# Kernel tuning notes

Measured on AMD Instinct MI355X. Metric: run time of the kernel, lower is better.

The kernel has to match this reference:

```python
import jax, jax.numpy as jnp
import numpy as np

TEM = 6  # forward hardcodes Tem=6 for index building; init default Tem=6 for weights


def _build_index(H, W, Tem):
    # Faithful port of _build_matrix_index: row edges per phase, col edges per phase,
    # then cross-phase edges linking corresponding pixels of adjacent phases.
    raw = jnp.arange(W, dtype=jnp.int32)[None, :] + jnp.arange(H, dtype=jnp.int32)[:, None] * W  # [H,W]
    pw = W // Tem
    phases = [raw[:, i * pw:(i + 1) * pw] for i in range(Tem)]
    rows = [jnp.stack([p[:-1, :], p[1:, :]], axis=2).reshape(-1, 2) for p in phases]
    cols = [jnp.stack([p[:, :-1], p[:, 1:]], axis=2).reshape(-1, 2) for p in phases]
    cross = [jnp.stack([phases[i], phases[i + 1]], axis=2).reshape(-1, 2) for i in range(Tem - 1)]
    return jnp.concatenate(rows + cols + cross, axis=0)  # [E,2]


def _build_weight_norm2(fm, Tem):
    # Faithful port of _build_feature_weight_norm2_distance, INCLUDING the original
    # per-phase [row,col] interleaved ordering (which differs from the index ordering).
    B, D, H, W = fm.shape
    pw = W // Tem
    phases = [fm[:, :, :, i * pw:(i + 1) * pw] for i in range(Tem)]
    ws = []
    for p in phases:
        wr = ((p[:, :, :-1, :] - p[:, :, 1:, :]) ** 2).sum(axis=1).reshape(B, -1)
        wc = ((p[:, :, :, :-1] - p[:, :, :, 1:]) ** 2).sum(axis=1).reshape(B, -1)
        ws.extend([wr, wc])
    for i in range(Tem - 1):
        ws.append(((phases[i] - phases[i + 1]) ** 2).sum(axis=1).reshape(B, -1))
    return jnp.concatenate(ws, axis=1)  # [B,E]


def _mst_single(u, v, w, V):
    # Vectorized Boruvka MST with pointer-jumping union-find (jit-compatible,
    # fixed round count >= ceil(log2 V)). Ties broken by a globally unique edge rank.
    E = u.shape[0]
    order = jnp.argsort(w)  # stable -> unique rank per edge
    rank = jnp.zeros(E, jnp.int32).at[order].set(jnp.arange(E, dtype=jnp.int32))
    n_rounds = int(np.ceil(np.log2(max(V, 2)))) + 1
    idx_v = jnp.arange(V, dtype=jnp.int32)

    def round_fn(carry, _):
        comp, mask = carry
        cu, cv = comp[u], comp[v]
        active = cu != cv
        key = jnp.where(active, rank, E)  # E = sentinel 'no edge'
        mk = jnp.minimum(jax.ops.segment_min(key, cu, num_segments=V),
                         jax.ops.segment_min(key, cv, num_segments=V))  # min rank per component
        has = mk < E
        sel = order[jnp.clip(mk, 0, E - 1)]  # chosen edge index per component
        a, b = cu[sel], cv[sel]
        other = jnp.where(a == idx_v, b, a)
        parent = jnp.where(has, other, idx_v)
        # break mutual 2-cycles: smaller-index component becomes root
        gp = parent[parent]
        parent = jnp.where((gp == idx_v) & (idx_v < parent), idx_v, parent)
        # full path compression via pointer jumping
        parent = jax.lax.while_loop(lambda p: jnp.any(p[p] != p), lambda p: p[p], parent)
        comp = parent[comp]
        mask = mask.at[jnp.where(has, sel, E)].set(True)  # slot E is scratch
        return (comp, mask), None

    comp0 = jnp.arange(V, dtype=jnp.int32)
    mask0 = jnp.zeros(E + 1, dtype=bool)
    (comp, mask), _ = jax.lax.scan(round_fn, (comp0, mask0), None, length=n_rounds)
    mask = mask[:E]
    # grid graph is connected -> exactly V-1 selected edges; emit sorted edge ids
    tree = jnp.sort(jnp.where(mask, jnp.arange(E, dtype=jnp.int32), E))[: V - 1]
    return tree  # [V-1] int32


def setup_inputs() -> dict:
    key = jax.random.key(0)
    guide_in = jax.random.normal(key, (4, 64, 288, 432), dtype=jnp.float32)
    return {"guide_in": guide_in}


def reference(guide_in):
    B, C, H, W = guide_in.shape
    V = H * W
    index = _build_index(H, W, TEM)  # [E,2], same for every batch element
    weight = _build_weight_norm2(guide_in, TEM)  # [B,E]
    u, v = index[:, 0], index[:, 1]
    tree = jax.vmap(lambda ww: _mst_single(u, v, ww, V))(weight)  # [B, V-1]
    return tree
```

## Files before the change

### kernel.cpp

```cpp
#include <hip/hip_runtime.h>
#include <cstdint>
#include <cstddef>

#define NB 4
#define NC 64
#define HH 288
#define WW 432
#define PW 72
#define NV (HH*WW)
#define R_PER ((HH-1)*PW)
#define C_PER (HH*(PW-1))
#define X_PER (HH*PW)
#define PAIRW (R_PER + C_PER)
#define ROWS_TOT (6*R_PER)
#define ROWCOL (6*PAIRW)
#define NE (ROWCOL + 5*X_PER)
#define NEB ((NE + 255)/256)
#define EPT 4
#define NEB4 ((NE + 1023)/1024)
#define NTREE (NV-1)
#define NROUNDS 18
#define CHUNK 4096
#define NCHUNK ((NE + CHUNK - 1)/CHUNK)
#define CSTR 32
#define SLB 128

typedef unsigned long long ull;

__device__ __forceinline__ void index_uv(int e, int& u, int& v) {
    if (e < ROWS_TOT) {
        int t = e / R_PER, l = e - t * R_PER;
        int h = l / PW, x = l - h * PW;
        u = h * WW + t * PW + x; v = u + WW;
    } else if (e < ROWCOL) {
        int q = e - ROWS_TOT;
        int t = q / C_PER, l = q - t * C_PER;
        int h = l / (PW-1), x = l - h * (PW-1);
        u = h * WW + t * PW + x; v = u + 1;
    } else {
        int q = e - ROWCOL;
        int t = q / X_PER, l = q - t * X_PER;
        int h = l / PW, x = l - h * PW;
        u = h * WW + t * PW + x; v = u + PW;
    }
}

__device__ __forceinline__ int rootOf2(const int* __restrict__ par, int c, int p) {
    while (true) {
        if (p == c) return c;
        int pp = par[p];
        if (pp == c) return c < p ? c : p;
        c = p; p = pp;
    }
}

__global__ __launch_bounds__(256) void init_kernel(int* comp, int* parent,
                                                   ull* minkey, unsigned char* mask,
                                                   int* cnt, int* found, int* done) {
    int i = blockIdx.x * 256 + threadIdx.x;
    int b = blockIdx.y;
    if (i < NV) {
        comp[(size_t)b*NV + i] = i;
        parent[(size_t)b*NV + i] = i;
        minkey[(size_t)b*NV + i] = ~0ULL;
    }
    if (i < NE) mask[(size_t)b*NE + i] = 0;
    if (b == 0 && i < 2*NB*CSTR) cnt[i] = 0;
    if (b == 0 && i < NB) { found[i] = 1; found[NB + i] = 0; done[i] = 0; }
}

__global__ __launch_bounds__(256) void key0_kernel(const float* __restrict__ fm,
                                                   ull* __restrict__ keys,
                                                   ull* __restrict__ minkey) {
    int i = blockIdx.x * 256 + threadIdx.x;
    int b = blockIdx.y;
    if (i >= NV) return;
    int h = i / WW, x = i - h * WW;
    int t = x / PW, xr = x - t * PW;
    bool hv = (h < HH-1);
    bool hh = (xr < PW-1);
    bool hx = (x < WW-PW);
    int ov = hv ? WW : 0;
    int oh = hh ? 1  : 0;
    int ox = hx ? PW : 0;
    const float* base = fm + (size_t)b * NC * NV + i;
    float sv = 0.f, sh_ = 0.f, sx = 0.f;
    #pragma unroll 8
    for (int ch = 0; ch < NC; ++ch) {
        const float* p = base + (size_t)ch * NV;
        float f0 = p[0];
        float dv = f0 - p[ov];
        float dh = f0 - p[oh];
        float dx = f0 - p[ox];
        sv += dv * dv; sh_ += dh * dh; sx += dx * dx;
    }
    ull* mk = minkey + (size_t)b * NV;
    ull* ky = keys + (size_t)b * NE;
    if (hv) {
        int e = t * PAIRW + h * PW + xr;
        ull k = ((ull)__float_as_uint(sv) << 32) | (unsigned int)e;
        ky[e] = k;
        int u, v; index_uv(e, u, v);
        atomicMin(&mk[u], k); atomicMin(&mk[v], k);
    }
    if (hh) {
        int e = t * PAIRW + R_PER + h * (PW-1) + xr;
        ull k = ((ull)__float_as_uint(sh_) << 32) | (unsigned int)e;
        ky[e] = k;
        int u, v; index_uv(e, u, v);
        atomicMin(&mk[u], k); atomicMin(&mk[v], k);
    }
    if (hx) {
        int e = ROWCOL + t * X_PER + h * PW + xr;
        ull k = ((ull)__float_as_uint(sx) << 32) | (unsigned int)e;
        ky[e] = k;
        int u, v; index_uv(e, u, v);
        atomicMin(&mk[u], k); atomicMin(&mk[v], k);
    }
}

__global__ __launch_bounds__(256) void scan_full_kernel(const ull* __restrict__ keys,
                                                        int* __restrict__ comp,
                                                        const int* __restrict__ parent,
                                                        ull* __restrict__ minkey,
                                                        int* __restrict__ list0,
                                                        int* __restrict__ cnt,
                                                        int* __restrict__ fCur) {
    const int tid = threadIdx.x;
    const int b = blockIdx.y;
    const int ebase = blockIdx.x * (256 * EPT) + tid;
    const size_t offV = (size_t)b * NV;
    const int* par = parent + offV;
    int* cmp = comp + offV;
    ull* mk = minkey + offV;
    const ull* ky = keys + (size_t)b * NE;

    int e[EPT], uu[EPT], vv[EPT], cu0[EPT], cv0[EPT], pu0[EPT], pv0[EPT];
    ull k[EPT];
    bool valid[EPT], live[EPT];
    #pragma unroll
    for (int j = 0; j < EPT; ++j) {
        e[j] = ebase + j * 256;
        valid[j] = e[j] < NE;
        int u = 0, v = 0;
        if (valid[j]) index_uv(e[j], u, v);
        uu[j] = u; vv[j] = v;
    }
    #pragma unroll
    for (int j = 0; j < EPT; ++j) {
        cu0[j] = valid[j] ? cmp[uu[j]] : 0;
        cv0[j] = valid[j] ? cmp[vv[j]] : 0;
        k[j]   = valid[j] ? ky[e[j]] : 0;
    }
    #pragma unroll
    for (int j = 0; j < EPT; ++j) {
        pu0[j] = valid[j] ? par[cu0[j]] : 0;
        pv0[j] = valid[j] ? par[cv0[j]] : 0;
    }
    #pragma unroll
    for (int j = 0; j < EPT; ++j) {
        live[j] = false;
        if (valid[j]) {
            int cu = rootOf2(par, cu0[j], pu0[j]);
            int cv = rootOf2(par, cv0[j], pv0[j]);
            if (cu0[j] != cu) cmp[uu[j]] = cu;
            if (cv0[j] != cv) cmp[vv[j]] = cv;
            live[j] = (cu != cv);
            if (live[j]) {
                if (k[j] < mk[cu]) atomicMin(&mk[cu], k[j]);
                if (k[j] < mk[cv]) atomicMin(&mk[cv], k[j]);
            }
        }
    }
    __shared__ int s_w[4];
    __shared__ int s_bcnt;
    __shared__ int s_gb;
    const int lane = tid & 63;
    const int wid = tid >> 6;
    ull wl[EPT]; int wcnt = 0;
    #pragma unroll
    for (int j = 0; j < EPT; ++j) { wl[j] = __ballot(live[j] ? 1 : 0); wcnt += __popcll(wl[j]); }
    if (tid == 0) s_bcnt = 0;
    __syncthreads();
    if (lane == 0) s_w[wid] = wcnt ? atomicAdd(&s_bcnt, wcnt) : 0;
    __syncthreads();
    if (tid == 0 && s_bcnt) {
        s_gb = atomicAdd(&cnt[b * CSTR], s_bcnt);
        fCur[b] = 1;
    }
    __syncthreads();
    int pre = 0;
    #pragma unroll
    for (int j = 0; j < EPT; ++j) {
        if (live[j]) {
            int pos = s_gb + s_w[wid] + pre + __popcll(wl[j] & ((1ull << lane) - 1));
            list0[(size_t)b * NE + pos] = e[j];
        }
        pre += __popcll(wl[j]);
    }
}

__global__ __launch_bounds__(256) void scan_list_kernel(const ull* __restrict__ keys,
                                                        int* __restrict__ comp,
                                                        const int* __restrict__ parent,
                                                        ull* __restrict__ minkey,
                                                        int* __restrict__ list0,
                                                        int* __restrict__ list1,
                                                        int* __restrict__ cnt,
                                                        int rpar,
                                                        int* __restrict__ fCur,
                                                        const int* __restrict__ done) {
    const int b = blockIdx.y;
    if (done[b]) return;
    const int tid = threadIdx.x;
    const int n = cnt[rpar * NB * CSTR + b * CSTR];
    int* cw = &cnt[(rpar ^ 1) * NB * CSTR + b * CSTR];
    const int* lr = (rpar ? list1 : list0) + (size_t)b * NE;
    int* lw = (rpar ? list0 : list1) + (size_t)b * NE;
    const size_t offV = (size_t)b * NV;
    const int* par = parent + offV;
    int* cmp = comp + offV;
    ull* mk = minkey + offV;
    const ull* ky = keys + (size_t)b * NE;

    const int stride = SLB * 256 * EPT;
    const int nIter = (n + stride - 1) / stride;
    const int lane = tid & 63;
    const int wid = tid >> 6;
    __shared__ int s_w[4];
    __shared__ int s_bcnt;
    __shared__ int s_gb;

    for (int it = 0; it < nIter; ++it) {
        const int ibase = it * stride + blockIdx.x * (256 * EPT) + tid;
        int e[EPT], uu[EPT], vv[EPT], cu0[EPT], cv0[EPT], pu0[EPT], pv0[EPT];
        ull k[EPT];
        bool valid[EPT], live[EPT];
        #pragma unroll
        for (int j = 0; j < EPT; ++j) {
            int i = ibase + j * 256;
            valid[j] = i < n;
            e[j] = valid[j] ? lr[i] : 0;
        }
        #pragma unroll
        for (int j = 0; j < EPT; ++j) {
            int u = 0, v = 0;
            if (valid[j]) index_uv(e[j], u, v);
            uu[j] = u; vv[j] = v;
        }
        #pragma unroll
        for (int j = 0; j < EPT; ++j) {
            cu0[j] = valid[j] ? cmp[uu[j]] : 0;
            cv0[j] = valid[j] ? cmp[vv[j]] : 0;
            k[j]   = valid[j] ? ky[e[j]] : 0;
        }
        #pragma unroll
        for (int j = 0; j < EPT; ++j) {
            pu0[j] = valid[j] ? par[cu0[j]] : 0;
            pv0[j] = valid[j] ? par[cv0[j]] : 0;
        }
        #pragma unroll
        for (int j = 0; j < EPT; ++j) {
            live[j] = false;
            if (valid[j]) {
                int cu = rootOf2(par, cu0[j], pu0[j]);
                int cv = rootOf2(par, cv0[j], pv0[j]);
                if (cu0[j] != cu) cmp[uu[j]] = cu;
                if (cv0[j] != cv) cmp[vv[j]] = cv;
                live[j] = (cu != cv);
                if (live[j]) {
                    if (k[j] < mk[cu]) atomicMin(&mk[cu], k[j]);
                    if (k[j] < mk[cv]) atomicMin(&mk[cv], k[j]);
                }
            }
        }
        ull wl[EPT]; int wcnt = 0;
        #pragma unroll
        for (int j = 0; j < EPT; ++j) { wl[j] = __ballot(live[j] ? 1 : 0); wcnt += __popcll(wl[j]); }
        if (tid == 0) s_bcnt = 0;
        __syncthreads();
        if (lane == 0) s_w[wid] = wcnt ? atomicAdd(&s_bcnt, wcnt) : 0;
        __syncthreads();
        if (tid == 0 && s_bcnt) {
            s_gb = atomicAdd(cw, s_bcnt);
            fCur[b] = 1;
        }
        __syncthreads();
        int pre = 0;
        #pragma unroll
        for (int j = 0; j < EPT; ++j) {
            if (live[j]) {
                int pos = s_gb + s_w[wid] + pre + __popcll(wl[j] & ((1ull << lane) - 1));
                lw[pos] = e[j];
            }
            pre += __popcll(wl[j]);
        }
    }
}

__global__ __launch_bounds__(256) void select_kernel(const int* __restrict__ comp,
                                                     int* __restrict__ parent,
                                                     ull* __restrict__ minkey,
                                                     unsigned char* __restrict__ mask,
                                                     const int* __restrict__ foundCur,
                                                     int* __restrict__ foundNext,
                                                     int* __restrict__ done,
                                                     int* __restrict__ cnt,
                                                     int zpar) {
    int gid = blockIdx.x * 256 + threadIdx.x;
    int b = blockIdx.y;
    int fc = foundCur[b];
    if (gid == 0) {
        foundNext[b] = 0;
        cnt[zpar * NB * CSTR + b * CSTR] = 0;
        if (fc == 0) done[b] = 1;
    }
    if (fc == 0) return;
    int c0 = gid * 4;
    if (c0 >= NV) return;
    size_t off = (size_t)b * NV;
    ulonglong4 kv = *reinterpret_cast<const ulonglong4*>(minkey + off + c0);
    int4 pv = *reinterpret_cast<const int4*>(parent + off + c0);
    ull kk[4] = {kv.x, kv.y, kv.z, kv.w};
    int pold[4] = {pv.x, pv.y, pv.z, pv.w};
    #pragma unroll
    for (int j = 0; j < 4; ++j) {
        int c = c0 + j;
        int pr = c;
        if (kk[j] != ~0ULL) {
            minkey[off + c] = ~0ULL;
            int e = (int)(kk[j] & 0xffffffffu);
            mask[(size_t)b * NE + e] = 1;
            int u, v; index_uv(e, u, v);
            int cu = comp[off + u], cv = comp[off + v];
            pr = (cu == c) ? cv : cu;
        }
        if (pold[j] != pr) parent[off + c] = pr;
    }
}

__global__ __launch_bounds__(256) void count_kernel(const unsigned char* __restrict__ mask,
                                                    int* __restrict__ counts) {
    int b = blockIdx.y, ck = blockIdx.x, t = threadIdx.x;
    const unsigned char* m = mask + (size_t)b * NE;
    int base_e = ck * CHUNK + t * 16;
    int cnt = 0;
    #pragma unroll
    for (int i = 0; i < 16; ++i) {
        int e = base_e + i;
        if (e < NE && m[e]) cnt++;
    }
    __shared__ int sh[256];
    sh[t] = cnt;
    __syncthreads();
    for (int o = 128; o > 0; o >>= 1) {
        if (t < o) sh[t] += sh[t + o];
        __syncthreads();
    }
    if (t == 0) counts[b * NCHUNK + ck] = sh[0];
}

__global__ __launch_bounds__(256) void write_kernel(const unsigned char* __restrict__ mask,
                                                    const int* __restrict__ counts,
                                                    int* __restrict__ out) {
    int b = blockIdx.y, ck = blockIdx.x, t = threadIdx.x;
    __shared__ int sh[256];
    __shared__ int shOff[128];
    shOff[t & 127] = 0;
    __syncthreads();
    if (t < NCHUNK && t < ck) shOff[t] = counts[b * NCHUNK + t];
    __syncthreads();
    for (int o = 64; o > 0; o >>= 1) {
        if (t < o) shOff[t] += shOff[t + o];
        __syncthreads();
    }
    int blockOff = shOff[0];

    const unsigned char* m = mask + (size_t)b * NE;
    int base_e = ck * CHUNK + t * 16;
    int cnt = 0;
    #pragma unroll
    for (int i = 0; i < 16; ++i) {
        int e = base_e + i;
        if (e < NE && m[e]) cnt++;
    }
    sh[t] = cnt;
    __syncthreads();
    for (int o = 1; o < 256; o <<= 1) {
        int v = 0;
        if (t >= o) v = sh[t - o];
        __syncthreads();
        sh[t] += v;
        __syncthreads();
    }
    int pos = blockOff + (sh[t] - cnt);
    for (int i = 0; i < 16; ++i) {
        int e = base_e + i;
        if (e < NE && m[e]) {
            if (pos < NTREE) out[(size_t)b * NTREE + pos] = e;
            pos++;
        }
    }
}

extern "C" void kernel_launch(void* const* d_in, const int* in_sizes, int n_in,
                              void* d_out, int out_size, void* d_ws, size_t ws_size,
                              hipStream_t stream) {
    const float* fm = (const float*)d_in[0];
    int* out = (int*)d_out;

    char* ws = (char*)d_ws;
    size_t off = 0;
    auto alloc = [&](size_t bytes) -> void* {
        void* p = ws + off;
        off += (bytes + 255) & ~(size_t)255;
        return p;
    };
    ull* keys    = (ull*)alloc((size_t)NB * NE * 8);
    ull* minkey  = (ull*)alloc((size_t)NB * NV * 8);
    int* comp    = (int*)alloc((size_t)NB * NV * 4);
    int* parent  = (int*)alloc((size_t)NB * NV * 4);
    unsigned char* mask = (unsigned char*)alloc((size_t)NB * NE);
    int* list0   = (int*)alloc((size_t)NB * NE * 4);
    int* list1   = (int*)alloc((size_t)NB * NE * 4);
    int* cnt     = (int*)alloc(2 * NB * CSTR * 4);
    int* counts  = (int*)alloc((size_t)NB * NCHUNK * 4);
    int* found   = (int*)alloc(2 * NB * 4);
    int* done    = (int*)alloc(NB * 4);

    dim3 blk(256);
    dim3 gE(NEB, NB);
    dim3 gE4(NEB4, NB);
    dim3 gV((NV + 255) / 256, NB);
    dim3 gVS((NV/4 + 255) / 256, NB);
    dim3 gL(SLB, NB);

    init_kernel<<<gE, blk, 0, stream>>>(comp, parent, minkey, mask, cnt, found, done);
    key0_kernel<<<gV, blk, 0, stream>>>(fm, keys, minkey);

    select_kernel<<<gVS, blk, 0, stream>>>(comp, parent, minkey, mask,
                                           found, found + NB, done, cnt, 0);
    scan_full_kernel<<<gE4, blk, 0, stream>>>(keys, comp, parent, minkey,
                                              list0, cnt, found + NB);
    select_kernel<<<gVS, blk, 0, stream>>>(comp, parent, minkey, mask,
                                           found + NB, found, done, cnt, 1);
    for (int r = 2; r < NROUNDS; ++r) {
        int* fCur  = found + (r & 1) * NB;
        int* fNext = found + ((r + 1) & 1) * NB;
        scan_list_kernel<<<gL, blk, 0, stream>>>(keys, comp, parent, minkey,
                                                 list0, list1, cnt, r & 1,
                                                 fCur, done);
        select_kernel<<<gVS, blk, 0, stream>>>(comp, parent, minkey, mask,
                                               fCur, fNext, done, cnt, r & 1);
    }

    count_kernel<<<dim3(NCHUNK, NB), blk, 0, stream>>>(mask, counts);
    write_kernel<<<dim3(NCHUNK, NB), blk, 0, stream>>>(mask, counts, out);
}
```

Baseline: 583.2 us.

## Run late Boruvka rounds in a single persistent per-batch block kernel

After round 6, the remaining Boruvka rounds run in one kernel with a single 512-thread block per batch element. That block loops over rounds internally and uses block barriers instead of launching a scan/select kernel pair per round. Roots that gain a minimum edge are recorded in a compact root buffer, so the select step walks only those roots instead of all vertices. This removes about 24 kernel launches and full-vertex select passes. In exchange, the tail runs on only 4 blocks, which is slow if many edges remain, and the fixed root-buffer capacity could overflow.

```diff
diff --git a/kernel.cpp b/kernel.cpp
--- a/kernel.cpp
+++ b/kernel.cpp
@@ -20,6 +20,9 @@
 #define NEB4 ((NE + 1023)/1024)
 #define NTREE (NV-1)
 #define NROUNDS 18
+#define TAIL_START 6
+#define TBLK 512
+#define RB_CAP 4096
 #define CHUNK 4096
 #define NCHUNK ((NE + CHUNK - 1)/CHUNK)
 #define CSTR 32
@@ -339,6 +342,122 @@
     }
 }
 
+__global__ __launch_bounds__(TBLK) void tail_kernel(const ull* __restrict__ keys,
+                                                    int* __restrict__ comp,
+                                                    int* __restrict__ parent,
+                                                    ull* __restrict__ minkey,
+                                                    unsigned char* __restrict__ mask,
+                                                    int* __restrict__ list0,
+                                                    int* __restrict__ list1,
+                                                    const int* __restrict__ cnt,
+                                                    int* __restrict__ rootbuf) {
+    const int b = blockIdx.x;
+    const int tid = threadIdx.x;
+    const int lane = tid & 63;
+    const int wid = tid >> 6;
+    const size_t offV = (size_t)b * NV;
+    int* cmp = comp + offV;
+    int* par = parent + offV;
+    ull* mk = minkey + offV;
+    const ull* ky = keys + (size_t)b * NE;
+    unsigned char* msk = mask + (size_t)b * NE;
+    int* la = list0 + (size_t)b * NE;
+    int* lb = list1 + (size_t)b * NE;
+    int* rb = rootbuf + (size_t)b * RB_CAP;
+
+    __shared__ int s_out;
+    __shared__ int s_nr;
+    __shared__ int s_wb[TBLK/64];
+
+    int rpar = TAIL_START & 1;
+    int n = cnt[rpar * NB * CSTR + b * CSTR];
+
+    for (int r = TAIL_START; r < NROUNDS && n > 0; ++r) {
+        const int* lr = rpar ? lb : la;
+        int* lw = rpar ? la : lb;
+        if (tid == 0) { s_out = 0; s_nr = 0; }
+        __syncthreads();
+        for (int base = 0; base < n; base += TBLK * EPT) {
+            int e[EPT], uu[EPT], vv[EPT], cu0[EPT], cv0[EPT], pu0[EPT], pv0[EPT];
+            ull k[EPT];
+            bool valid[EPT], live[EPT];
+            #pragma unroll
+            for (int j = 0; j < EPT; ++j) {
+                int i = base + tid + j * TBLK;
+                valid[j] = i < n;
+                e[j] = valid[j] ? lr[i] : 0;
+            }
+            #pragma unroll
+            for (int j = 0; j < EPT; ++j) {
+                int u = 0, v = 0;
+                if (valid[j]) index_uv(e[j], u, v);
+                uu[j] = u; vv[j] = v;
+            }
+            #pragma unroll
+            for (int j = 0; j < EPT; ++j) {
+                cu0[j] = valid[j] ? cmp[uu[j]] : 0;
+                cv0[j] = valid[j] ? cmp[vv[j]] : 0;
+                k[j]   = valid[j] ? ky[e[j]] : 0;
+            }
+            #pragma unroll
+            for (int j = 0; j < EPT; ++j) {
+                pu0[j] = valid[j] ? par[cu0[j]] : 0;
+                pv0[j] = valid[j] ? par[cv0[j]] : 0;
+            }
+            #pragma unroll
+            for (int j = 0; j < EPT; ++j) {
+                live[j] = false;
+                if (valid[j]) {
+                    int cu = rootOf2(par, cu0[j], pu0[j]);
+                    int cv = rootOf2(par, cv0[j], pv0[j]);
+                    if (cu0[j] != cu) cmp[uu[j]] = cu;
+                    if (cv0[j] != cv) cmp[vv[j]] = cv;
+                    live[j] = (cu != cv);
+                    if (live[j]) {
+                        if (k[j] < mk[cu]) {
+                            ull old = atomicMin(&mk[cu], k[j]);
+                            if (old == ~0ULL) rb[atomicAdd(&s_nr, 1)] = cu;
+                        }
+                        if (k[j] < mk[cv]) {
+                            ull old = atomicMin(&mk[cv], k[j]);
+                            if (old == ~0ULL) rb[atomicAdd(&s_nr, 1)] = cv;
+                        }
+                    }
+                }
+            }
+            ull wl[EPT]; int wcnt = 0;
+            #pragma unroll
+            for (int j = 0; j < EPT; ++j) { wl[j] = __ballot(live[j] ? 1 : 0); wcnt += __popcll(wl[j]); }
+            if (lane == 0) s_wb[wid] = wcnt ? atomicAdd(&s_out, wcnt) : 0;
+            int pre = 0;
+            #pragma unroll
+            for (int j = 0; j < EPT; ++j) {
+                if (live[j]) {
+                    int pos = s_wb[wid] + pre + __popcll(wl[j] & ((1ull << lane) - 1));
+                    lw[pos] = e[j];
+                }
+                pre += __popcll(wl[j]);
+            }
+        }
+        __syncthreads();
+        int nout = s_out;
+        int nr = s_nr;
+        for (int i = tid; i < nr; i += TBLK) {
+            int c = rb[i];
+            ull k = mk[c];
+            mk[c] = ~0ULL;
+            int e = (int)(k & 0xffffffffu);
+            msk[e] = 1;
+            int u, v; index_uv(e, u, v);
+            int cu = cmp[u], cv = cmp[v];
+            par[c] = (cu == c) ? cv : cu;
+        }
+        __syncthreads();
+        n = nout;
+        rpar ^= 1;
+    }
+}
+
 __global__ __launch_bounds__(256) void count_kernel(const unsigned char* __restrict__ mask,
                                                     int* __restrict__ counts) {
     int b = blockIdx.y, ck = blockIdx.x, t = threadIdx.x;
@@ -424,6 +543,7 @@
     int* list0   = (int*)alloc((size_t)NB * NE * 4);
     int* list1   = (int*)alloc((size_t)NB * NE * 4);
     int* cnt     = (int*)alloc(2 * NB * CSTR * 4);
+    int* rootbuf = (int*)alloc((size_t)NB * RB_CAP * 4);
     int* counts  = (int*)alloc((size_t)NB * NCHUNK * 4);
     int* found   = (int*)alloc(2 * NB * 4);
     int* done    = (int*)alloc(NB * 4);
@@ -444,7 +564,7 @@
                                               list0, cnt, found + NB);
     select_kernel<<<gVS, blk, 0, stream>>>(comp, parent, minkey, mask,
                                            found + NB, found, done, cnt, 1);
-    for (int r = 2; r < NROUNDS; ++r) {
+    for (int r = 2; r < TAIL_START; ++r) {
         int* fCur  = found + (r & 1) * NB;
         int* fNext = found + ((r + 1) & 1) * NB;
         scan_list_kernel<<<gL, blk, 0, stream>>>(keys, comp, parent, minkey,
@@ -453,6 +573,9 @@
         select_kernel<<<gVS, blk, 0, stream>>>(comp, parent, minkey, mask,
                                                fCur, fNext, done, cnt, r & 1);
     }
+    tail_kernel<<<dim3(NB), dim3(TBLK), 0, stream>>>(keys, comp, parent, minkey,
+                                                     mask, list0, list1, cnt,
+                                                     rootbuf);
 
     count_kernel<<<dim3(NCHUNK, NB), blk, 0, stream>>>(mask, counts);
     write_kernel<<<dim3(NCHUNK, NB), blk, 0, stream>>>(mask, counts, out);
```

New measurement: 887.2 us. +52.1%, slower.

## Replace dense per-vertex select pass with sparse root-list select

Applied to the files above, without the earlier changes.

Scan kernels now record each component root whose minkey first changes from the sentinel into a compacted per-batch list, using the old value returned by atomicMin. A sparse select kernel then processes only those roots instead of sweeping every vertex each round. The found/done early-exit flags are removed and the round count is lowered by one. This relies on the root list fitting in RLCAP entries after round 1, and on the fixed round count still being enough for the MST to finish.

```diff
diff --git a/kernel.cpp b/kernel.cpp
--- a/kernel.cpp
+++ b/kernel.cpp
@@ -19,11 +19,13 @@
 #define EPT 4
 #define NEB4 ((NE + 1023)/1024)
 #define NTREE (NV-1)
-#define NROUNDS 18
+#define NROUNDS 17
 #define CHUNK 4096
 #define NCHUNK ((NE + CHUNK - 1)/CHUNK)
 #define CSTR 32
 #define SLB 128
+#define SSB 64
+#define RLCAP 65536
 
 typedef unsigned long long ull;
 
@@ -56,7 +58,7 @@
 
 __global__ __launch_bounds__(256) void init_kernel(int* comp, int* parent,
                                                    ull* minkey, unsigned char* mask,
-                                                   int* cnt, int* found, int* done) {
+                                                   int* cnt, int* rlc) {
     int i = blockIdx.x * 256 + threadIdx.x;
     int b = blockIdx.y;
     if (i < NV) {
@@ -65,8 +67,7 @@
         minkey[(size_t)b*NV + i] = ~0ULL;
     }
     if (i < NE) mask[(size_t)b*NE + i] = 0;
-    if (b == 0 && i < 2*NB*CSTR) cnt[i] = 0;
-    if (b == 0 && i < NB) { found[i] = 1; found[NB + i] = 0; done[i] = 0; }
+    if (b == 0 && i < 2*NB*CSTR) { cnt[i] = 0; rlc[i] = 0; }
 }
 
 __global__ __launch_bounds__(256) void key0_kernel(const float* __restrict__ fm,
@@ -119,13 +120,63 @@
     }
 }
 
+__global__ __launch_bounds__(256) void select0_kernel(const int* __restrict__ comp,
+                                                      int* __restrict__ parent,
+                                                      ull* __restrict__ minkey,
+                                                      unsigned char* __restrict__ mask) {
+    int gid = blockIdx.x * 256 + threadIdx.x;
+    int b = blockIdx.y;
+    int c0 = gid * 4;
+    if (c0 >= NV) return;
+    size_t off = (size_t)b * NV;
+    ulonglong4 kv = *reinterpret_cast<const ulonglong4*>(minkey + off + c0);
+    ull kk[4] = {kv.x, kv.y, kv.z, kv.w};
+    #pragma unroll
+    for (int j = 0; j < 4; ++j) {
+        int c = c0 + j;
+        if (kk[j] != ~0ULL) {
+            minkey[off + c] = ~0ULL;
+            int e = (int)(kk[j] & 0xffffffffu);
+            mask[(size_t)b * NE + e] = 1;
+            int u, v; index_uv(e, u, v);
+            int cu = comp[off + u], cv = comp[off + v];
+            parent[off + c] = (cu == c) ? cv : cu;
+        }
+    }
+}
+
+#define EMIT_ROOTS(fcu, fcv, cuA, cvA, rlW, rlcSlot)                          \
+    {                                                                         \
+        int tot = 0;                                                          \
+        _Pragma("unroll")                                                     \
+        for (int j = 0; j < EPT; ++j) {                                       \
+            tot += __popcll(__ballot(fcu[j] ? 1 : 0));                        \
+            tot += __popcll(__ballot(fcv[j] ? 1 : 0));                        \
+        }                                                                     \
+        int base_ = 0;                                                        \
+        if (lane == 0 && tot) base_ = atomicAdd(rlcSlot, tot);                \
+        base_ = __shfl(base_, 0);                                             \
+        ull ltm = (1ull << lane) - 1;                                         \
+        int pre_ = 0;                                                         \
+        _Pragma("unroll")                                                     \
+        for (int j = 0; j < EPT; ++j) {                                       \
+            ull bu = __ballot(fcu[j] ? 1 : 0);                                \
+            if (fcu[j]) rlW[base_ + pre_ + __popcll(bu & ltm)] = cuA[j];      \
+            pre_ += __popcll(bu);                                             \
+            ull bv = __ballot(fcv[j] ? 1 : 0);                                \
+            if (fcv[j]) rlW[base_ + pre_ + __popcll(bv & ltm)] = cvA[j];      \
+            pre_ += __popcll(bv);                                             \
+        }                                                                     \
+    }
+
 __global__ __launch_bounds__(256) void scan_full_kernel(const ull* __restrict__ keys,
                                                         int* __restrict__ comp,
                                                         const int* __restrict__ parent,
                                                         ull* __restrict__ minkey,
                                                         int* __restrict__ list0,
                                                         int* __restrict__ cnt,
-                                                        int* __restrict__ fCur) {
+                                                        int* __restrict__ rlWb,
+                                                        int* __restrict__ rlcW) {
     const int tid = threadIdx.x;
     const int b = blockIdx.y;
     const int ebase = blockIdx.x * (256 * EPT) + tid;
@@ -134,10 +185,12 @@
     int* cmp = comp + offV;
     ull* mk = minkey + offV;
     const ull* ky = keys + (size_t)b * NE;
+    int* rlW = rlWb + (size_t)b * RLCAP;
 
     int e[EPT], uu[EPT], vv[EPT], cu0[EPT], cv0[EPT], pu0[EPT], pv0[EPT];
+    int cuA[EPT], cvA[EPT];
     ull k[EPT];
-    bool valid[EPT], live[EPT];
+    bool valid[EPT], live[EPT], fcu[EPT], fcv[EPT];
     #pragma unroll
     for (int j = 0; j < EPT; ++j) {
         e[j] = ebase + j * 256;
@@ -159,24 +212,26 @@
     }
     #pragma unroll
     for (int j = 0; j < EPT; ++j) {
-        live[j] = false;
+        live[j] = false; fcu[j] = false; fcv[j] = false; cuA[j] = 0; cvA[j] = 0;
         if (valid[j]) {
             int cu = rootOf2(par, cu0[j], pu0[j]);
             int cv = rootOf2(par, cv0[j], pv0[j]);
             if (cu0[j] != cu) cmp[uu[j]] = cu;
             if (cv0[j] != cv) cmp[vv[j]] = cv;
+            cuA[j] = cu; cvA[j] = cv;
             live[j] = (cu != cv);
             if (live[j]) {
-                if (k[j] < mk[cu]) atomicMin(&mk[cu], k[j]);
-                if (k[j] < mk[cv]) atomicMin(&mk[cv], k[j]);
+                if (k[j] < mk[cu]) fcu[j] = (atomicMin(&mk[cu], k[j]) == ~0ULL);
+                if (k[j] < mk[cv]) fcv[j] = (atomicMin(&mk[cv], k[j]) == ~0ULL);
             }
         }
     }
+    const int lane = tid & 63;
+    const int wid = tid >> 6;
+    EMIT_ROOTS(fcu, fcv, cuA, cvA, rlW, &rlcW[b * CSTR])
     __shared__ int s_w[4];
     __shared__ int s_bcnt;
     __shared__ int s_gb;
-    const int lane = tid & 63;
-    const int wid = tid >> 6;
     ull wl[EPT]; int wcnt = 0;
     #pragma unroll
     for (int j = 0; j < EPT; ++j) { wl[j] = __ballot(live[j] ? 1 : 0); wcnt += __popcll(wl[j]); }
@@ -184,10 +239,7 @@
     __syncthreads();
     if (lane == 0) s_w[wid] = wcnt ? atomicAdd(&s_bcnt, wcnt) : 0;
     __syncthreads();
-    if (tid == 0 && s_bcnt) {
-        s_gb = atomicAdd(&cnt[b * CSTR], s_bcnt);
-        fCur[b] = 1;
-    }
+    if (tid == 0 && s_bcnt) s_gb = atomicAdd(&cnt[b * CSTR], s_bcnt);
     __syncthreads();
     int pre = 0;
     #pragma unroll
@@ -208,10 +260,9 @@
                                                         int* __restrict__ list1,
                                                         int* __restrict__ cnt,
                                                         int rpar,
-                                                        int* __restrict__ fCur,
-                                                        const int* __restrict__ done) {
+                                                        int* __restrict__ rlWb,
+                                                        int* __restrict__ rlcW) {
     const int b = blockIdx.y;
-    if (done[b]) return;
     const int tid = threadIdx.x;
     const int n = cnt[rpar * NB * CSTR + b * CSTR];
     int* cw = &cnt[(rpar ^ 1) * NB * CSTR + b * CSTR];
@@ -222,6 +273,7 @@
     int* cmp = comp + offV;
     ull* mk = minkey + offV;
     const ull* ky = keys + (size_t)b * NE;
+    int* rlW = rlWb + (size_t)b * RLCAP;
 
     const int stride = SLB * 256 * EPT;
     const int nIter = (n + stride - 1) / stride;
@@ -234,8 +286,9 @@
     for (int it = 0; it < nIter; ++it) {
         const int ibase = it * stride + blockIdx.x * (256 * EPT) + tid;
         int e[EPT], uu[EPT], vv[EPT], cu0[EPT], cv0[EPT], pu0[EPT], pv0[EPT];
+        int cuA[EPT], cvA[EPT];
         ull k[EPT];
-        bool valid[EPT], live[EPT];
+        bool valid[EPT], live[EPT], fcu[EPT], fcv[EPT];
         #pragma unroll
         for (int j = 0; j < EPT; ++j) {
             int i = ibase + j * 256;
@@ -261,19 +314,21 @@
         }
         #pragma unroll
         for (int j = 0; j < EPT; ++j) {
-            live[j] = false;
+            live[j] = false; fcu[j] = false; fcv[j] = false; cuA[j] = 0; cvA[j] = 0;
             if (valid[j]) {
                 int cu = rootOf2(par, cu0[j], pu0[j]);
                 int cv = rootOf2(par, cv0[j], pv0[j]);
                 if (cu0[j] != cu) cmp[uu[j]] = cu;
                 if (cv0[j] != cv) cmp[vv[j]] = cv;
+                cuA[j] = cu; cvA[j] = cv;
                 live[j] = (cu != cv);
                 if (live[j]) {
-                    if (k[j] < mk[cu]) atomicMin(&mk[cu], k[j]);
-                    if (k[j] < mk[cv]) atomicMin(&mk[cv], k[j]);
+                    if (k[j] < mk[cu]) fcu[j] = (atomicMin(&mk[cu], k[j]) == ~0ULL);
+                    if (k[j] < mk[cv]) fcv[j] = (atomicMin(&mk[cv], k[j]) == ~0ULL);
                 }
             }
         }
+        EMIT_ROOTS(fcu, fcv, cuA, cvA, rlW, &rlcW[b * CSTR])
         ull wl[EPT]; int wcnt = 0;
         #pragma unroll
         for (int j = 0; j < EPT; ++j) { wl[j] = __ballot(live[j] ? 1 : 0); wcnt += __popcll(wl[j]); }
@@ -281,10 +336,7 @@
         __syncthreads();
         if (lane == 0) s_w[wid] = wcnt ? atomicAdd(&s_bcnt, wcnt) : 0;
         __syncthreads();
-        if (tid == 0 && s_bcnt) {
-            s_gb = atomicAdd(cw, s_bcnt);
-            fCur[b] = 1;
-        }
+        if (tid == 0 && s_bcnt) s_gb = atomicAdd(cw, s_bcnt);
         __syncthreads();
         int pre = 0;
         #pragma unroll
@@ -298,44 +350,31 @@
     }
 }
 
-__global__ __launch_bounds__(256) void select_kernel(const int* __restrict__ comp,
-                                                     int* __restrict__ parent,
-                                                     ull* __restrict__ minkey,
-                                                     unsigned char* __restrict__ mask,
-                                                     const int* __restrict__ foundCur,
-                                                     int* __restrict__ foundNext,
-                                                     int* __restrict__ done,
-                                                     int* __restrict__ cnt,
-                                                     int zpar) {
-    int gid = blockIdx.x * 256 + threadIdx.x;
-    int b = blockIdx.y;
-    int fc = foundCur[b];
-    if (gid == 0) {
-        foundNext[b] = 0;
-        cnt[zpar * NB * CSTR + b * CSTR] = 0;
-        if (fc == 0) done[b] = 1;
-    }
-    if (fc == 0) return;
-    int c0 = gid * 4;
-    if (c0 >= NV) return;
-    size_t off = (size_t)b * NV;
-    ulonglong4 kv = *reinterpret_cast<const ulonglong4*>(minkey + off + c0);
-    int4 pv = *reinterpret_cast<const int4*>(parent + off + c0);
-    ull kk[4] = {kv.x, kv.y, kv.z, kv.w};
-    int pold[4] = {pv.x, pv.y, pv.z, pv.w};
-    #pragma unroll
-    for (int j = 0; j < 4; ++j) {
-        int c = c0 + j;
-        int pr = c;
-        if (kk[j] != ~0ULL) {
-            minkey[off + c] = ~0ULL;
-            int e = (int)(kk[j] & 0xffffffffu);
-            mask[(size_t)b * NE + e] = 1;
-            int u, v; index_uv(e, u, v);
-            int cu = comp[off + u], cv = comp[off + v];
-            pr = (cu == c) ? cv : cu;
-        }
-        if (pold[j] != pr) parent[off + c] = pr;
+__global__ __launch_bounds__(256) void select_sparse_kernel(const int* __restrict__ comp,
+                                                            int* __restrict__ parent,
+                                                            ull* __restrict__ minkey,
+                                                            unsigned char* __restrict__ mask,
+                                                            const int* __restrict__ rlRb,
+                                                            const int* __restrict__ rlcCur,
+                                                            int* __restrict__ cntZ,
+                                                            int* __restrict__ rlcZ) {
+    const int b = blockIdx.y;
+    if (blockIdx.x == 0 && threadIdx.x == 0) {
+        cntZ[b * CSTR] = 0;
+        rlcZ[b * CSTR] = 0;
+    }
+    const int nr = rlcCur[b * CSTR];
+    const int* rlR = rlRb + (size_t)b * RLCAP;
+    const size_t off = (size_t)b * NV;
+    for (int i = blockIdx.x * 256 + threadIdx.x; i < nr; i += SSB * 256) {
+        int c = rlR[i];
+        ull k = minkey[off + c];
+        minkey[off + c] = ~0ULL;
+        int e = (int)(k & 0xffffffffu);
+        mask[(size_t)b * NE + e] = 1;
+        int u, v; index_uv(e, u, v);
+        int cu = comp[off + u], cv = comp[off + v];
+        parent[off + c] = (cu == c) ? cv : cu;
     }
 }
 
@@ -424,9 +463,9 @@
     int* list0   = (int*)alloc((size_t)NB * NE * 4);
     int* list1   = (int*)alloc((size_t)NB * NE * 4);
     int* cnt     = (int*)alloc(2 * NB * CSTR * 4);
+    int* rl      = (int*)alloc(2 * (size_t)NB * RLCAP * 4);
+    int* rlc     = (int*)alloc(2 * NB * CSTR * 4);
     int* counts  = (int*)alloc((size_t)NB * NCHUNK * 4);
-    int* found   = (int*)alloc(2 * NB * 4);
-    int* done    = (int*)alloc(NB * 4);
 
     dim3 blk(256);
     dim3 gE(NEB, NB);
@@ -434,24 +473,31 @@
     dim3 gV((NV + 255) / 256, NB);
     dim3 gVS((NV/4 + 255) / 256, NB);
     dim3 gL(SLB, NB);
-
-    init_kernel<<<gE, blk, 0, stream>>>(comp, parent, minkey, mask, cnt, found, done);
+    dim3 gS(SSB, NB);
+
+    init_kernel<<<gE, blk, 0, stream>>>(comp, parent, minkey, mask, cnt, rlc);
     key0_kernel<<<gV, blk, 0, stream>>>(fm, keys, minkey);
-
-    select_kernel<<<gVS, blk, 0, stream>>>(comp, parent, minkey, mask,
-                                           found, found + NB, done, cnt, 0);
+    select0_kernel<<<gVS, blk, 0, stream>>>(comp, parent, minkey, mask);
     scan_full_kernel<<<gE4, blk, 0, stream>>>(keys, comp, parent, minkey,
-                                              list0, cnt, found + NB);
-    select_kernel<<<gVS, blk, 0, stream>>>(comp, parent, minkey, mask,
-                                           found + NB, found, done, cnt, 1);
+                                              list0, cnt,
+                                              rl + (size_t)NB * RLCAP,
+                                              rlc + NB * CSTR);
+    select_sparse_kernel<<<gS, blk, 0, stream>>>(comp, parent, minkey, mask,
+                                                 rl + (size_t)NB * RLCAP,
+                                                 rlc + NB * CSTR,
+                                                 cnt + NB * CSTR,
+                                                 rlc);
     for (int r = 2; r < NROUNDS; ++r) {
-        int* fCur  = found + (r & 1) * NB;
-        int* fNext = found + ((r + 1) & 1) * NB;
+        int rp = r & 1, ro = (r + 1) & 1;
         scan_list_kernel<<<gL, blk, 0, stream>>>(keys, comp, parent, minkey,
-                                                 list0, list1, cnt, r & 1,
-                                                 fCur, done);
-        select_kernel<<<gVS, blk, 0, stream>>>(comp, parent, minkey, mask,
-                                               fCur, fNext, done, cnt, r & 1);
+                                                 list0, list1, cnt, rp,
+                                                 rl + (size_t)rp * NB * RLCAP,
+                                                 rlc + rp * NB * CSTR);
+        select_sparse_kernel<<<gS, blk, 0, stream>>>(comp, parent, minkey, mask,
+                                                     rl + (size_t)rp * NB * RLCAP,
+                                                     rlc + rp * NB * CSTR,
+                                                     cnt + rp * NB * CSTR,
+                                                     rlc + ro * NB * CSTR);
     }
 
     count_kernel<<<dim3(NCHUNK, NB), blk, 0, stream>>>(mask, counts);
```

Result: faster. 571.2 us (-2.0%).
